# Performance work log

Hardware: AMD Instinct MI355X
Metric: run time of the kernel (lower is better)

Reference implementation:

```python
import jax, jax.numpy as jnp
import numpy as np

# --- quantization-format simulation helpers (numpy, used only in setup) ---
FP4_GRID = np.array([0.0, 0.5, 1.0, 1.5, 2.0, 3.0, 4.0, 6.0], np.float32)  # e2m1 magnitudes
FP4_MID = (FP4_GRID[:-1] + FP4_GRID[1:]) / 2.0
E4M3_MAX = 448.0


def _round_e4m3(x):
    """Round-to-nearest onto an fp8 e4m3-like grid (3 mantissa bits, clamp to 448)."""
    x = np.clip(x, -E4M3_MAX, E4M3_MAX)
    a = np.abs(x)
    e = np.clip(np.floor(np.log2(np.maximum(a, 1e-12))), -6, 8)
    step = np.exp2(e - 3)
    return (np.round(x / step) * step).astype(np.float32)


def _quant_fp4_mag(a):
    """Nearest e2m1 magnitude for non-negative a."""
    idx = np.searchsorted(FP4_MID, a)
    return FP4_GRID[idx]


def setup_inputs() -> dict:
    rng = np.random.default_rng(0)
    IN, OUT, P = 4096, 4096, 8
    k_fp8 = ((IN // P + 127) // 128) * 128   # 512
    k_fp4 = IN - k_fp8                       # 3584

    w = (rng.standard_normal((OUT, IN)) * 0.023).astype(np.float32)
    w4 = w[:, :k_fp4]
    w8 = w[:, k_fp4:]

    # --- NVFP4 quantization: per-128 fp32 outer scale, per-16 e4m3 inner scale ---
    b128 = w4.reshape(OUT, k_fp4 // 128, 128)
    os = np.maximum(np.abs(b128).max(-1) / (6.0 * E4M3_MAX), 1e-12).astype(np.float32)  # (OUT, k4/128)
    b16 = w4.reshape(OUT, k_fp4 // 128, 8, 16)
    is_q = _round_e4m3(np.abs(b16).max(-1) / 6.0 / os[..., None])  # (OUT, k4/128, 8)
    denom = np.maximum(is_q * os[..., None], 1e-12)
    q4 = np.sign(b16) * _quant_fp4_mag(np.abs(b16) / denom[..., None])
    w_q_fp4 = q4.reshape(OUT, k_fp4).astype(np.float32)
    w_is_fp4 = is_q.reshape(OUT, k_fp4 // 16).astype(np.float32)
    w_os_fp4 = os

    # --- fp8 quantization: per-32 e8m0 (power-of-2) scale ---
    b32 = w8.reshape(OUT, k_fp8 // 32, 32)
    amax = np.maximum(np.abs(b32).max(-1), 1e-12)
    s8 = np.exp2(np.ceil(np.log2(amax / E4M3_MAX))).astype(np.float32)
    w_q_fp8 = _round_e4m3(b32 / s8[..., None]).reshape(OUT, k_fp8)
    w_s_fp8 = s8

    # --- dequantized transposed weight buffer (as the module precomputes) ---
    w4_dq = w_q_fp4 * np.repeat(w_is_fp4, 16, 1) * np.repeat(w_os_fp4, 128, 1)
    w8_dq = w_q_fp8 * np.repeat(w_s_fp8, 32, 1)
    w_t = np.ascontiguousarray(np.concatenate([w4_dq, w8_dq], 1).T)  # (IN, OUT)

    x = rng.standard_normal((8192, IN)).astype(np.float32)
    return {
        "x": jnp.asarray(x),
        "w_q_fp4": jnp.asarray(w_q_fp4),
        "w_os_fp4": jnp.asarray(w_os_fp4),
        "w_is_fp4": jnp.asarray(w_is_fp4),
        "w_t": jnp.asarray(w_t),
        "w_q_fp8": jnp.asarray(w_q_fp8),
        "w_s_fp8": jnp.asarray(w_s_fp8),
    }


def reference(x, w_q_fp4, w_os_fp4, w_is_fp4, w_t, w_q_fp8, w_s_fp8):
    OUT = w_q_fp4.shape[0]
    k4 = w_q_fp4.shape[1]
    # fused dequant of fp4 partition: value * inner_scale(per 16) * outer_scale(per 128)
    w4 = (w_q_fp4.reshape(OUT, k4 // 16, 16) * w_is_fp4[..., None]).reshape(OUT, k4)
    w4 = (w4.reshape(OUT, k4 // 128, 128) * w_os_fp4[..., None]).reshape(OUT, k4)
    # dequant of fp8 partition: value * e8m0 scale (per 32)
    k8 = w_q_fp8.shape[1]
    w8 = (w_q_fp8.reshape(OUT, k8 // 32, 32) * w_s_fp8[..., None]).reshape(OUT, k8)
    W = jnp.concatenate([w4, w8], axis=1)  # (OUT, IN)
    return x @ W.T  # (tokens, OUT)
```

## Files before the change

kernel.cpp:

```cpp
#include <hip/hip_runtime.h>
#include <stdint.h>

#define K_DIM 4096
#define N_DIM 4096
#define KS_DIM (K_DIM / 32)
#define NT_DIM (N_DIM / 16)

typedef __attribute__((ext_vector_type(8))) short s16x8;
typedef __attribute__((ext_vector_type(4))) float f32x4;

static __device__ __forceinline__ unsigned short f32_to_bf16(float f) {
    union { float f; unsigned int u; } v; v.f = f;
    unsigned int u = v.u;
    u += 0x7FFFu + ((u >> 16) & 1u);
    return (unsigned short)(u >> 16);
}


extern "C" __global__ void pack_x_k(const float* __restrict__ in,
                                    unsigned short* __restrict__ out, int MT) {
    int wid = blockIdx.x * 4 + (threadIdx.x >> 6);
    int lane = threadIdx.x & 63;
    int mt = wid % MT, ks = wid / MT;
    int r = lane & 15, q = lane >> 4;
    const float* src = in + (size_t)(mt * 16 + r) * K_DIM + ks * 32 + q * 8;
    float4 a = *(const float4*)src;
    float4 b = *(const float4*)(src + 4);
    s16x8 o;
    o[0] = (short)f32_to_bf16(a.x); o[1] = (short)f32_to_bf16(a.y);
    o[2] = (short)f32_to_bf16(a.z); o[3] = (short)f32_to_bf16(a.w);
    o[4] = (short)f32_to_bf16(b.x); o[5] = (short)f32_to_bf16(b.y);
    o[6] = (short)f32_to_bf16(b.z); o[7] = (short)f32_to_bf16(b.w);
    *(s16x8*)(out + ((size_t)wid * 64 + lane) * 8) = o;
}

extern "C" __global__ void pack_w_k(const float* __restrict__ in,
                                    unsigned short* __restrict__ out) {
    __shared__ __align__(16) unsigned short tile[64][72];
    int n0 = blockIdx.x * 64, k0 = blockIdx.y * 64;
    int t = threadIdx.x;
    int tr = t >> 4, tc = (t & 15) * 4;
#pragma unroll
    for (int i = 0; i < 4; ++i) {
        int k = tr + i * 16;
        float4 v = *(const float4*)(in + (size_t)(k0 + k) * N_DIM + n0 + tc);
        tile[tc + 0][k] = f32_to_bf16(v.x);
        tile[tc + 1][k] = f32_to_bf16(v.y);
        tile[tc + 2][k] = f32_to_bf16(v.z);
        tile[tc + 3][k] = f32_to_bf16(v.w);
    }
    __syncthreads();
    int f = t >> 5, h = f >> 2, ntl = f & 3;
    int ks = blockIdx.y * 2 + h;
    int nt = blockIdx.x * 4 + ntl;
    unsigned short* dst = out + ((size_t)(ks * NT_DIM + nt) * 64) * 8;
#pragma unroll
    for (int u = 0; u < 2; ++u) {
        int c = (t & 31) * 2 + u;
        int r = c & 15, q = c >> 4;
        s16x8 o = *(const s16x8*)&tile[ntl * 16 + r][h * 32 + q * 8];
        *(s16x8*)(dst + (size_t)c * 8) = o;
    }
}

__device__ __forceinline__ void async_cp16(const unsigned short* g, unsigned short* l) {
    __builtin_amdgcn_global_load_lds(
        (const __attribute__((address_space(1))) unsigned int*)g,
        (__attribute__((address_space(3))) unsigned int*)l, 16, 0, 0);
}

extern "C" __global__ __launch_bounds__(256)
void gemm_pk(const unsigned short* __restrict__ Ap,
             const unsigned short* __restrict__ Bp,
             float* __restrict__ C, int M) {
    const int N = N_DIM;
    const int MT = M >> 4;
    __shared__ __align__(16) unsigned short sA[8 * 512];
    const int tid = threadIdx.x;
    const int wave = tid >> 6, lane = tid & 63;
    const int wm = (wave >> 1) * 64, wn = (wave & 1) * 64;
    f32x4 acc[4][4] = {};

    const unsigned short* gA =
        Ap + ((size_t)(blockIdx.y * 8 + wave * 2) * 64 + lane) * 8;
    unsigned short* lA = sA + (wave * 2) * 512;
    const unsigned short* gB =
        Bp + ((size_t)(blockIdx.x * 8 + (wave & 1) * 4) * 64 + lane) * 8;
    const unsigned short* fA = sA + (wave >> 1) * 4 * 512 + lane * 8;

    for (int ks = 0; ks < KS_DIM; ++ks) {
        __syncthreads();
        async_cp16(gA, lA);
        async_cp16(gA + 512, lA + 512);
        gA += (size_t)MT * 512;
        s16x8 bf[4];
#pragma unroll
        for (int j = 0; j < 4; ++j)
            bf[j] = *(const s16x8*)(gB + (size_t)j * 512);
        gB += (size_t)NT_DIM * 512;
        __syncthreads();
        s16x8 af[4];
#pragma unroll
        for (int i = 0; i < 4; ++i)
            af[i] = *(const s16x8*)(fA + i * 512);
#pragma unroll
        for (int i = 0; i < 4; ++i)
#pragma unroll
            for (int j = 0; j < 4; ++j)
                acc[i][j] = __builtin_amdgcn_mfma_f32_16x16x32_bf16(
                    af[i], bf[j], acc[i][j], 0, 0, 0);
    }
    const size_t tileM = (size_t)blockIdx.y * 128, tileN = (size_t)blockIdx.x * 128;
#pragma unroll
    for (int i = 0; i < 4; ++i)
#pragma unroll
        for (int j = 0; j < 4; ++j) {
            size_t row = tileM + wm + i * 16 + (lane >> 4) * 4;
            size_t col = tileN + wn + j * 16 + (lane & 15);
#pragma unroll
            for (int r = 0; r < 4; ++r)
                C[(row + r) * N + col] = acc[i][j][r];
        }
}

extern "C" __global__ __launch_bounds__(256)
void gemm_f32_k(const float* __restrict__ X,
                const float* __restrict__ Wt,
                float* __restrict__ C, int M) {
    const int K = K_DIM, N = N_DIM;
    __shared__ __align__(16) unsigned short sA[128 * 32];
    __shared__ __align__(16) unsigned short sB[128 * 32];
    const int tid = threadIdx.x;
    const int wave = tid >> 6, lane = tid & 63;
    const int wm = (wave >> 1) * 64, wn = (wave & 1) * 64;
    const size_t tileM = (size_t)blockIdx.y * 128, tileN = (size_t)blockIdx.x * 128;
    const int frow = lane & 15, fcol = (lane >> 4) * 8;
    f32x4 acc[4][4] = {};
    for (int k0 = 0; k0 < K; k0 += 32) {
        __syncthreads();
#pragma unroll
        for (int it = 0; it < 4; ++it) {
            int idx = it * 256 + tid;
            int m = idx >> 3, c4 = (idx & 7) * 4;
            float4 v = *(const float4*)(X + (tileM + m) * (size_t)K + k0 + c4);
            sA[m * 32 + c4 + 0] = f32_to_bf16(v.x);
            sA[m * 32 + c4 + 1] = f32_to_bf16(v.y);
            sA[m * 32 + c4 + 2] = f32_to_bf16(v.z);
            sA[m * 32 + c4 + 3] = f32_to_bf16(v.w);
        }
#pragma unroll
        for (int it = 0; it < 16; ++it) {
            int idx = it * 256 + tid;
            int k = idx >> 7, n = idx & 127;
            float v = Wt[(size_t)(k0 + k) * N + tileN + n];
            sB[n * 32 + k] = f32_to_bf16(v);
        }
        __syncthreads();
        s16x8 af[4], bfr[4];
#pragma unroll
        for (int i = 0; i < 4; ++i)
            af[i] = *(const s16x8*)(sA + (wm + i * 16 + frow) * 32 + fcol);
#pragma unroll
        for (int j = 0; j < 4; ++j)
            bfr[j] = *(const s16x8*)(sB + (wn + j * 16 + frow) * 32 + fcol);
#pragma unroll
        for (int i = 0; i < 4; ++i)
#pragma unroll
            for (int j = 0; j < 4; ++j)
                acc[i][j] = __builtin_amdgcn_mfma_f32_16x16x32_bf16(
                    af[i], bfr[j], acc[i][j], 0, 0, 0);
    }
#pragma unroll
    for (int i = 0; i < 4; ++i)
#pragma unroll
        for (int j = 0; j < 4; ++j) {
            size_t row = tileM + wm + i * 16 + (lane >> 4) * 4;
            size_t col = tileN + wn + j * 16 + (lane & 15);
#pragma unroll
            for (int r = 0; r < 4; ++r)
                C[(row + r) * N + col] = acc[i][j][r];
        }
}

extern "C" void kernel_launch(void* const* d_in, const int* in_sizes, int n_in,
                              void* d_out, int out_size, void* d_ws, size_t ws_size,
                              hipStream_t stream) {
    const float* x   = (const float*)d_in[0];
    const float* w_t = (const float*)d_in[4];
    float* out = (float*)d_out;
    const int K = K_DIM, N = N_DIM;
    const int M = in_sizes[0] / K;
    const int MT = M / 16;
    const size_t need = (size_t)M * K * 2 + (size_t)N * K * 2;
    if (ws_size >= need) {
        unsigned short* ap = (unsigned short*)d_ws;
        unsigned short* bp = ap + (size_t)M * K;
        int nwave = KS_DIM * MT;
        hipLaunchKernelGGL(pack_x_k, dim3(nwave / 4), dim3(256), 0, stream,
                           x, ap, MT);
        hipLaunchKernelGGL(pack_w_k, dim3(N / 64, K / 64), dim3(256), 0, stream,
                           w_t, bp);
        hipLaunchKernelGGL(gemm_pk, dim3(N / 128, M / 128), dim3(256), 0, stream,
                           ap, bp, out, M);
    } else {
        hipLaunchKernelGGL(gemm_f32_k, dim3(N / 128, M / 128), dim3(256), 0, stream,
                           x, w_t, out, M);
    }
}
```

Baseline: 627.9 us.

## Rewrite packed GEMM as 256x256 tile with 4-stage async LDS pipeline

The packed bf16 GEMM moves from 128x128 tiles with 256 threads to 256x256 tiles with 512 threads. A 4-slot LDS ring buffer is filled by async global-to-LDS copies three stages ahead, gated by explicit vmcnt waits and one barrier per k-step. It also adds a grid swizzle for L2 locality and raises wave priority around the MFMA block. The larger per-wave accumulator tile and the 128 KB of LDS limit occupancy and raise register pressure.

```diff
diff --git a/kernel.cpp b/kernel.cpp
--- a/kernel.cpp
+++ b/kernel.cpp
@@ -69,57 +69,105 @@
         (__attribute__((address_space(3))) unsigned int*)l, 16, 0, 0);
 }
 
-extern "C" __global__ __launch_bounds__(256)
+#define SLOTS 4
+#define SLOT_SHORTS (32 * 512)
+
+__device__ __forceinline__ void sbar() {
+    __builtin_amdgcn_sched_barrier(0);
+    __builtin_amdgcn_s_barrier();
+    __builtin_amdgcn_sched_barrier(0);
+}
+
+template <int VM>
+__device__ __forceinline__ void wait_vm() {
+    if constexpr (VM == 8)      asm volatile("s_waitcnt vmcnt(8)" ::: "memory");
+    else if constexpr (VM == 4) asm volatile("s_waitcnt vmcnt(4)" ::: "memory");
+    else                        asm volatile("s_waitcnt vmcnt(0)" ::: "memory");
+    __builtin_amdgcn_sched_barrier(0);
+}
+
+#define BODY(T, VM, STAGE)                                                  \
+  {                                                                         \
+    wait_vm<VM>();                                                          \
+    sbar();                                                                 \
+    if (STAGE) {                                                            \
+      unsigned short* d = lds + (((T) + 3) & 3) * SLOT_SHORTS + dsOff;      \
+      _Pragma("unroll")                                                     \
+      for (int fi = 0; fi < 4; ++fi)                                        \
+        async_cp16(gstage + fi * 512, d + fi * 512);                        \
+      gstage += strideS;                                                    \
+    }                                                                       \
+    const unsigned short* a = lds + ((T) & 3) * SLOT_SHORTS + aOff;         \
+    const unsigned short* b = lds + ((T) & 3) * SLOT_SHORTS + bOff;         \
+    s16x8 af[8], bf[4];                                                     \
+    _Pragma("unroll")                                                       \
+    for (int i = 0; i < 8; ++i) af[i] = *(const s16x8*)(a + i * 512);       \
+    _Pragma("unroll")                                                       \
+    for (int j = 0; j < 4; ++j) bf[j] = *(const s16x8*)(b + j * 512);       \
+    __builtin_amdgcn_s_setprio(1);                                          \
+    _Pragma("unroll")                                                       \
+    for (int i = 0; i < 8; ++i)                                             \
+      _Pragma("unroll")                                                     \
+      for (int j = 0; j < 4; ++j)                                           \
+        acc[i][j] = __builtin_amdgcn_mfma_f32_16x16x32_bf16(                \
+            af[i], bf[j], acc[i][j], 0, 0, 0);                              \
+    __builtin_amdgcn_s_setprio(0);                                          \
+  }
+
+extern "C" __global__ __launch_bounds__(512, 2)
 void gemm_pk(const unsigned short* __restrict__ Ap,
              const unsigned short* __restrict__ Bp,
              float* __restrict__ C, int M) {
-    const int N = N_DIM;
+    __shared__ __align__(16) unsigned short lds[SLOTS * SLOT_SHORTS];
     const int MT = M >> 4;
-    __shared__ __align__(16) unsigned short sA[8 * 512];
     const int tid = threadIdx.x;
     const int wave = tid >> 6, lane = tid & 63;
-    const int wm = (wave >> 1) * 64, wn = (wave & 1) * 64;
-    f32x4 acc[4][4] = {};
-
-    const unsigned short* gA =
-        Ap + ((size_t)(blockIdx.y * 8 + wave * 2) * 64 + lane) * 8;
-    unsigned short* lA = sA + (wave * 2) * 512;
-    const unsigned short* gB =
-        Bp + ((size_t)(blockIdx.x * 8 + (wave & 1) * 4) * 64 + lane) * 8;
-    const unsigned short* fA = sA + (wave >> 1) * 4 * 512 + lane * 8;
-
-    for (int ks = 0; ks < KS_DIM; ++ks) {
-        __syncthreads();
-        async_cp16(gA, lA);
-        async_cp16(gA + 512, lA + 512);
-        gA += (size_t)MT * 512;
-        s16x8 bf[4];
-#pragma unroll
-        for (int j = 0; j < 4; ++j)
-            bf[j] = *(const s16x8*)(gB + (size_t)j * 512);
-        gB += (size_t)NT_DIM * 512;
-        __syncthreads();
-        s16x8 af[4];
-#pragma unroll
-        for (int i = 0; i < 4; ++i)
-            af[i] = *(const s16x8*)(fA + i * 512);
-#pragma unroll
-        for (int i = 0; i < 4; ++i)
-#pragma unroll
-            for (int j = 0; j < 4; ++j)
-                acc[i][j] = __builtin_amdgcn_mfma_f32_16x16x32_bf16(
-                    af[i], bf[j], acc[i][j], 0, 0, 0);
-    }
-    const size_t tileM = (size_t)blockIdx.y * 128, tileN = (size_t)blockIdx.x * 128;
-#pragma unroll
-    for (int i = 0; i < 4; ++i)
+
+    const int nwg = gridDim.x;
+    const int cpx = nwg >> 3;
+    const int swz = (blockIdx.x & 7) * cpx + (blockIdx.x >> 3);
+    const int bn = swz & (N_DIM / 256 - 1);
+    const int bm = swz >> 4;
+
+    const int wm2 = wave >> 2;
+    const int wn4 = wave & 3;
+    const int fr0 = (wave & 3) * 4;
+
+    const unsigned short* gstage = wm2
+        ? Bp + (((size_t)bn * 16 + fr0) * 64 + lane) * 8
+        : Ap + (((size_t)bm * 16 + fr0) * 64 + lane) * 8;
+    const size_t strideS = (size_t)(wm2 ? NT_DIM : MT) * 512;
+    const int dsOff = (wm2 * 16 + fr0) * 512;
+
+    const int aOff = (wm2 * 8) * 512 + lane * 8;
+    const int bOff = (16 + wn4 * 4) * 512 + lane * 8;
+
+    f32x4 acc[8][4] = {};
+
+#pragma unroll
+    for (int t = 0; t < SLOTS - 1; ++t) {
+        unsigned short* d = lds + t * SLOT_SHORTS + dsOff;
+#pragma unroll
+        for (int fi = 0; fi < 4; ++fi)
+            async_cp16(gstage + fi * 512, d + fi * 512);
+        gstage += strideS;
+    }
+
+    for (int t = 0; t < KS_DIM - 2; ++t)
+        BODY(t, 8, (t + 3 < KS_DIM));
+    BODY(KS_DIM - 2, 4, false);
+    BODY(KS_DIM - 1, 0, false);
+
+    const size_t tileM = (size_t)bm * 256, tileN = (size_t)bn * 256;
+#pragma unroll
+    for (int i = 0; i < 8; ++i)
 #pragma unroll
         for (int j = 0; j < 4; ++j) {
-            size_t row = tileM + wm + i * 16 + (lane >> 4) * 4;
-            size_t col = tileN + wn + j * 16 + (lane & 15);
+            size_t row = tileM + wm2 * 128 + i * 16 + (lane >> 4) * 4;
+            size_t col = tileN + wn4 * 64 + j * 16 + (lane & 15);
 #pragma unroll
             for (int r = 0; r < 4; ++r)
-                C[(row + r) * N + col] = acc[i][j][r];
+                C[(row + r) * N_DIM + col] = acc[i][j][r];
         }
 }
 
@@ -192,7 +240,7 @@
     const int M = in_sizes[0] / K;
     const int MT = M / 16;
     const size_t need = (size_t)M * K * 2 + (size_t)N * K * 2;
-    if (ws_size >= need) {
+    if (ws_size >= need && (M % 256) == 0) {
         unsigned short* ap = (unsigned short*)d_ws;
         unsigned short* bp = ap + (size_t)M * K;
         int nwave = KS_DIM * MT;
@@ -200,8 +248,8 @@
                            x, ap, MT);
         hipLaunchKernelGGL(pack_w_k, dim3(N / 64, K / 64), dim3(256), 0, stream,
                            w_t, bp);
-        hipLaunchKernelGGL(gemm_pk, dim3(N / 128, M / 128), dim3(256), 0, stream,
-                           ap, bp, out, M);
+        hipLaunchKernelGGL(gemm_pk, dim3((M / 256) * (N / 256)), dim3(512), 0,
+                           stream, ap, bp, out, M);
     } else {
         hipLaunchKernelGGL(gemm_f32_k, dim3(N / 128, M / 128), dim3(256), 0, stream,
                            x, w_t, out, M);
```

After: 533.4 us. 15.0% less time.
